# Performance work log

Hardware: AMD Instinct MI355X
Metric: run time of the kernel (lower is better)

The kernel has to match this reference:

```python
import jax, jax.numpy as jnp
import numpy as np

NUM_HEADS = 8
EPS = 1e-9


def setup_inputs() -> dict:
    key = jax.random.key(0)
    ks = jax.random.split(key, 8)
    B, N, D = 2, 2048, 512
    s = 1.0 / np.sqrt(D)
    x = jax.random.normal(ks[0], (B, N, D), dtype=jnp.float32)
    adjacency = jax.random.uniform(ks[1], (B, N, N), dtype=jnp.float32)
    # Linear weights stored as (in, out) so application is x @ W + b
    W_q = jax.random.normal(ks[2], (D, D), dtype=jnp.float32) * s
    W_k = jax.random.normal(ks[3], (D, D), dtype=jnp.float32) * s
    W_v = jax.random.normal(ks[4], (D, D), dtype=jnp.float32) * s
    b_q = jnp.zeros((D,), jnp.float32)
    b_k = jnp.zeros((D,), jnp.float32)
    b_v = jnp.zeros((D,), jnp.float32)
    # soul_gate: Linear(2D -> 1); weight stored as flat (2D,), bias scalar
    w_g = jax.random.normal(ks[5], (2 * D,), dtype=jnp.float32) * (1.0 / np.sqrt(2 * D))
    b_g = jnp.zeros((), jnp.float32)
    return {"x": x, "adjacency": adjacency, "W_q": W_q, "b_q": b_q,
            "W_k": W_k, "b_k": b_k, "W_v": W_v, "b_v": b_v,
            "w_g": w_g, "b_g": b_g}


def reference(x, adjacency, W_q, b_q, W_k, b_k, W_v, b_v, w_g, b_g):
    B, N, D = x.shape
    H = NUM_HEADS
    hd = D // H
    Q = (x @ W_q + b_q).reshape(B, N, H, hd)
    K = (x @ W_k + b_k).reshape(B, N, H, hd)
    V = (x @ W_v + b_v).reshape(B, N, H, hd)
    scores = jnp.einsum('bihd,bjhd->bhij', Q, K) / jnp.sqrt(jnp.float32(hd))
    # soul_gate(cat[x_i, x_j]) is linear, so it decomposes exactly:
    # bias[b,i,j] = x[b,i]@w_g[:D] + x[b,j]@w_g[D:] + b_g  (same math, no (B,N,N,2D) tensor)
    a = x @ w_g[:D]          # (B, N) contribution of x_i
    c = x @ w_g[D:]          # (B, N) contribution of x_j
    soul_bias = a[:, :, None] + c[:, None, :] + b_g   # (B, N, N)
    scores = scores + (soul_bias + jnp.log(adjacency + EPS))[:, None, :, :]
    attn = jax.nn.softmax(scores, axis=-1)            # (B, H, N, N)
    out = jnp.einsum('bhij,bjhd->bihd', attn, V).reshape(B, N, D)
    return out + x
```

## Files before the change

kernel.cpp:

```cpp
#include <hip/hip_runtime.h>
#include <hip/hip_bf16.h>

typedef __bf16 bf16x8 __attribute__((ext_vector_type(8)));
typedef float f32x4 __attribute__((ext_vector_type(4)));
typedef unsigned short u16x8 __attribute__((ext_vector_type(8)));

#define LOG2E 1.44269504f

__device__ __forceinline__ unsigned short f2bu(float f) {
    __hip_bfloat16 h = __float2bfloat16(f);
    unsigned short u;
    __builtin_memcpy(&u, &h, 2);
    return u;
}

__device__ __forceinline__ float fexp2(float x) {
#if __has_builtin(__builtin_amdgcn_exp2f)
    return __builtin_amdgcn_exp2f(x);
#else
    return __expf(x * 0.69314718f);
#endif
}

__device__ __forceinline__ float bu2f(unsigned short u) {
    unsigned int v = ((unsigned int)u) << 16;
    float f;
    __builtin_memcpy(&f, &v, 4);
    return f;
}

#define GLDS16(gp, lp) __builtin_amdgcn_global_load_lds( \
    (const __attribute__((address_space(1))) unsigned int*)(gp), \
    (__attribute__((address_space(3))) unsigned int*)(lp), 16, 0, 0)

#define OFF_QS  0u
#define OFF_KB  4194304u
#define OFF_VT  8388608u
#define OFF_CV  12582912u
#define OFF_XB  12599296u
#define OFF_WT  16793600u
#define OFF_MQ  18366464u
#define OFF_PO  35143680u
#define OFF_PL  51920896u

__global__ void k_prepwt(const float* __restrict__ x, const float* __restrict__ wg,
                         const float* __restrict__ w0, const float* __restrict__ w1,
                         const float* __restrict__ w2,
                         unsigned short* __restrict__ xb, float* __restrict__ cv2,
                         unsigned short* __restrict__ wt) {
    if (blockIdx.x < 1024) {
        int row = blockIdx.x * 4 + (threadIdx.x >> 6);
        int l = threadIdx.x & 63;
        const float4* xr = reinterpret_cast<const float4*>(x + (size_t)row * 512);
        float4 a = xr[l * 2], b2 = xr[l * 2 + 1];
        ushort4 o0, o1;
        o0.x = f2bu(a.x);  o0.y = f2bu(a.y);  o0.z = f2bu(a.z);  o0.w = f2bu(a.w);
        o1.x = f2bu(b2.x); o1.y = f2bu(b2.y); o1.z = f2bu(b2.z); o1.w = f2bu(b2.w);
        ushort4* dst = reinterpret_cast<ushort4*>(xb + (size_t)row * 512);
        dst[l * 2] = o0; dst[l * 2 + 1] = o1;
        const float4* wr = reinterpret_cast<const float4*>(wg + 512);
        float4 g0 = wr[l * 2], g1 = wr[l * 2 + 1];
        float s = a.x * g0.x + a.y * g0.y + a.z * g0.z + a.w * g0.w
                + b2.x * g1.x + b2.y * g1.y + b2.z * g1.z + b2.w * g1.w;
#pragma unroll
        for (int off = 32; off >= 1; off >>= 1) s += __shfl_xor(s, off, 64);
        if (l == 0) cv2[row] = fexp2((s - 8.0f) * LOG2E);
    } else {
        int bid2 = blockIdx.x - 1024;
        int z = bid2 >> 6, yy = bid2 & 63;
        int k0 = (yy >> 3) * 64, n0 = (yy & 7) * 64;
        const float* W = (z == 0) ? w0 : ((z == 1) ? w1 : w2);
        __shared__ float T[64][65];
        int c = threadIdx.x & 63, r0 = threadIdx.x >> 6;
#pragma unroll
        for (int i = 0; i < 16; i++) { int r = r0 + i * 4; T[r][c] = W[(k0 + r) * 512 + n0 + c]; }
        __syncthreads();
        unsigned short* Wt = wt + z * (512 * 512);
#pragma unroll
        for (int i = 0; i < 16; i++) { int a = r0 + i * 4; Wt[(n0 + a) * 512 + k0 + c] = f2bu(T[c][a]); }
    }
}

__global__ __launch_bounds__(256) void k_mid(
    const float* __restrict__ adj, const float* __restrict__ cv2,
    unsigned short* __restrict__ mq,
    const unsigned short* __restrict__ xb, const unsigned short* __restrict__ wt,
    const float* __restrict__ bq, const float* __restrict__ bk, const float* __restrict__ bv,
    unsigned short* __restrict__ Qs, unsigned short* __restrict__ Kb,
    unsigned short* __restrict__ Vt) {
    if (blockIdx.x < 8192) {
        int blk = blockIdx.x;
        int bic = blk >> 5, jt = blk & 31;
        int b = bic >> 7, ic = bic & 127;
        int t = threadIdx.x;
        int l = t >> 2, mt = t & 3, q = l >> 4, cl = l & 15;
        int j0 = jt * 64 + 16 * mt + q * 4;
        const float4 av = *reinterpret_cast<const float4*>(
            adj + ((size_t)(b * 2048 + ic * 16 + cl)) * 2048 + j0);
        const float4 cv = *reinterpret_cast<const float4*>(cv2 + b * 2048 + j0);
        ushort4 o;
        o.x = f2bu((av.x + 1e-9f) * cv.x);
        o.y = f2bu((av.y + 1e-9f) * cv.y);
        o.z = f2bu((av.z + 1e-9f) * cv.z);
        o.w = f2bu((av.w + 1e-9f) * cv.w);
        *reinterpret_cast<ushort4*>(mq + (size_t)bic * 32768 + jt * 1024 + l * 16 + mt * 4) = o;
        return;
    }
    int gid = blockIdx.x - 8192;
    int bx = gid & 63, by = (gid >> 6) & 3, z = gid >> 8;
    __shared__ __align__(16) unsigned short As[64 * 32];
    __shared__ __align__(16) unsigned short Bs[128 * 32];
    const unsigned short* Wt = wt + z * (512 * 512);
    const float* bias = (z == 0) ? bq : ((z == 1) ? bk : bv);
    float scale = (z == 0) ? (0.125f * LOG2E) : 1.0f;
    int m0 = bx * 64, n0 = by * 128;
    int tid = threadIdx.x, w = tid >> 6, l = tid & 63;
    int q = l >> 4, cl = l & 15;
    f32x4 acc[8];
#pragma unroll
    for (int nt = 0; nt < 8; nt++)
#pragma unroll
        for (int r = 0; r < 4; r++) acc[nt][r] = 0.f;
    int arow = l >> 2, ach = (l & 3) * 8;
    for (int k0 = 0; k0 < 512; k0 += 32) {
        GLDS16(xb + (size_t)(m0 + w * 16 + arow) * 512 + k0 + ach, As + w * 512);
#pragma unroll
        for (int e = 0; e < 2; e++)
            GLDS16(Wt + (size_t)(n0 + w * 32 + e * 16 + arow) * 512 + k0 + ach, Bs + w * 1024 + e * 512);
        __syncthreads();
        bf16x8 af = *reinterpret_cast<const bf16x8*>(As + (w * 16 + cl) * 32 + q * 8);
#pragma unroll
        for (int nt = 0; nt < 8; nt++) {
            bf16x8 bf = *reinterpret_cast<const bf16x8*>(Bs + (nt * 16 + cl) * 32 + q * 8);
            acc[nt] = __builtin_amdgcn_mfma_f32_16x16x32_bf16(af, bf, acc[nt], 0, 0, 0);
        }
        __syncthreads();
    }
    if (z == 2) {
        int n_ = (m0 + w * 16 + q * 4) & 2047;
        int b_ = (m0 + w * 16) >> 11;
#pragma unroll
        for (int nt = 0; nt < 8; nt++) {
            int col = n0 + nt * 16 + cl;
            int h_ = col >> 6, d_ = col & 63;
            float bv_ = bias[col];
            ushort4 o;
            o.x = f2bu(acc[nt][0] + bv_); o.y = f2bu(acc[nt][1] + bv_);
            o.z = f2bu(acc[nt][2] + bv_); o.w = f2bu(acc[nt][3] + bv_);
            *reinterpret_cast<ushort4*>(Vt + ((size_t)((b_ * 8 + h_) * 64 + d_)) * 2048 + n_) = o;
        }
    } else {
        unsigned short* Cout = (z == 0) ? Qs : Kb;
#pragma unroll
        for (int nt = 0; nt < 8; nt++) {
            int col = n0 + nt * 16 + cl;
            float bv_ = bias[col];
#pragma unroll
            for (int r = 0; r < 4; r++) {
                int row = m0 + w * 16 + q * 4 + r;
                Cout[(size_t)row * 512 + col] = f2bu((acc[nt][r] + bv_) * scale);
            }
        }
    }
}

__global__ __launch_bounds__(256, 3) void k_attn(
    const unsigned short* __restrict__ Qs, const unsigned short* __restrict__ Kb,
    const unsigned short* __restrict__ Vt, const unsigned short* __restrict__ mq,
    unsigned short* __restrict__ PO, float* __restrict__ PL) {
    __shared__ __align__(16) unsigned short Ks[2][4096];
    __shared__ __align__(16) unsigned short Vs[2][4096];
    __shared__ __align__(16) unsigned short PA[4][32 * 72];
    int bid = blockIdx.x;
    int h = bid >> 7, b = (bid >> 6) & 1, ig = (bid >> 2) & 15, js = bid & 3;
    int tid = threadIdx.x, w = tid >> 6, l = tid & 63, q = l >> 4, cl = l & 15;
    int bh = b * 8 + h;
    int ic0 = ig * 8 + w * 2;

    bf16x8 qf[2][2];
#pragma unroll
    for (int rc = 0; rc < 2; rc++) {
        const unsigned short* qp = Qs + (size_t)(b * 2048 + ig * 128 + w * 32 + rc * 16 + cl) * 512 + h * 64 + q * 8;
        qf[rc][0] = *reinterpret_cast<const bf16x8*>(qp);
        qf[rc][1] = *reinterpret_cast<const bf16x8*>(qp + 32);
    }
    bf16x8 ones;
#pragma unroll
    for (int i = 0; i < 8; i++) { unsigned short o1 = 0x3F80; __builtin_memcpy(((unsigned short*)&ones) + i, &o1, 2); }

    f32x4 O[2][4];
    f32x4 Osum[2];
#pragma unroll
    for (int rc = 0; rc < 2; rc++) {
#pragma unroll
        for (int nt = 0; nt < 4; nt++)
#pragma unroll
            for (int r = 0; r < 4; r++) O[rc][nt][r] = 0.f;
#pragma unroll
        for (int r = 0; r < 4; r++) Osum[rc][r] = 0.f;
    }

    const unsigned short* Kh = Kb + (size_t)b * 2048 * 512 + h * 64;
    const unsigned short* Vh = Vt + ((size_t)bh * 64) * 2048;
    const unsigned short* mb0 = mq + (size_t)(b * 128 + ic0) * 32768 + l * 16 + (size_t)(js * 8) * 1024;
    const unsigned short* mb1 = mb0 + 32768;
    unsigned short* pw = &PA[w][0];
    int lrow = l >> 2, lch = (l & 3) * 8;
    int jb0 = js * 512;

#pragma unroll
    for (int e = 0; e < 2; e++) {
        int c = w * 2 + e, kk = c >> 2, r16 = (c & 3) * 16;
        GLDS16(Kh + (size_t)(jb0 + r16 + lrow) * 512 + kk * 32 + lch, &Ks[0][kk * 2048 + r16 * 32]);
        GLDS16(Vh + (size_t)(r16 + lrow) * 2048 + jb0 + kk * 32 + lch, &Vs[0][kk * 2048 + r16 * 32]);
    }

    for (int t = 0; t < 8; t++) {
        int bufi = t & 1;
        __syncthreads();
        if (t < 7) {
            int jb = jb0 + (t + 1) * 64;
#pragma unroll
            for (int e = 0; e < 2; e++) {
                int c = w * 2 + e, kk = c >> 2, r16 = (c & 3) * 16;
                GLDS16(Kh + (size_t)(jb + r16 + lrow) * 512 + kk * 32 + lch, &Ks[bufi ^ 1][kk * 2048 + r16 * 32]);
                GLDS16(Vh + (size_t)(r16 + lrow) * 2048 + jb + kk * 32 + lch, &Vs[bufi ^ 1][kk * 2048 + r16 * 32]);
            }
        }
        u16x8 mc[2][2];
        {
            size_t off = (size_t)t * 1024;
            mc[0][0] = *reinterpret_cast<const u16x8*>(mb0 + off);
            mc[0][1] = *reinterpret_cast<const u16x8*>(mb0 + off + 8);
            mc[1][0] = *reinterpret_cast<const u16x8*>(mb1 + off);
            mc[1][1] = *reinterpret_cast<const u16x8*>(mb1 + off + 8);
        }
        f32x4 S[2][4];
#pragma unroll
        for (int rc = 0; rc < 2; rc++)
#pragma unroll
            for (int mt = 0; mt < 4; mt++)
#pragma unroll
                for (int r = 0; r < 4; r++) S[rc][mt][r] = 0.f;
#pragma unroll
        for (int mt = 0; mt < 4; mt++) {
            bf16x8 kf0 = *reinterpret_cast<const bf16x8*>(&Ks[bufi][(16 * mt + cl) * 32 + q * 8]);
            bf16x8 kf1 = *reinterpret_cast<const bf16x8*>(&Ks[bufi][2048 + (16 * mt + cl) * 32 + q * 8]);
#pragma unroll
            for (int rc = 0; rc < 2; rc++) {
                S[rc][mt] = __builtin_amdgcn_mfma_f32_16x16x32_bf16(kf0, qf[rc][0], S[rc][mt], 0, 0, 0);
                S[rc][mt] = __builtin_amdgcn_mfma_f32_16x16x32_bf16(kf1, qf[rc][1], S[rc][mt], 0, 0, 0);
            }
        }
#pragma unroll
        for (int rc = 0; rc < 2; rc++) {
#pragma unroll
            for (int mt = 0; mt < 4; mt++) {
                float p0 = fexp2(S[rc][mt][0]) * bu2f((mt < 2) ? mc[rc][0][mt * 4 + 0] : mc[rc][1][(mt - 2) * 4 + 0]);
                float p1 = fexp2(S[rc][mt][1]) * bu2f((mt < 2) ? mc[rc][0][mt * 4 + 1] : mc[rc][1][(mt - 2) * 4 + 1]);
                float p2 = fexp2(S[rc][mt][2]) * bu2f((mt < 2) ? mc[rc][0][mt * 4 + 2] : mc[rc][1][(mt - 2) * 4 + 2]);
                float p3 = fexp2(S[rc][mt][3]) * bu2f((mt < 2) ? mc[rc][0][mt * 4 + 3] : mc[rc][1][(mt - 2) * 4 + 3]);
                ushort4 o;
                o.x = f2bu(p0); o.y = f2bu(p1); o.z = f2bu(p2); o.w = f2bu(p3);
                *reinterpret_cast<ushort4*>(pw + rc * (16 * 72) + cl * 72 + 16 * mt + q * 4) = o;
            }
        }
#pragma unroll
        for (int jc = 0; jc < 2; jc++) {
            bf16x8 pf0 = *reinterpret_cast<const bf16x8*>(pw + cl * 72 + jc * 32 + q * 8);
            bf16x8 pf1 = *reinterpret_cast<const bf16x8*>(pw + 16 * 72 + cl * 72 + jc * 32 + q * 8);
#pragma unroll
            for (int nt = 0; nt < 4; nt++) {
                bf16x8 vf = *reinterpret_cast<const bf16x8*>(&Vs[bufi][jc * 2048 + (16 * nt + cl) * 32 + q * 8]);
                O[0][nt] = __builtin_amdgcn_mfma_f32_16x16x32_bf16(pf0, vf, O[0][nt], 0, 0, 0);
                O[1][nt] = __builtin_amdgcn_mfma_f32_16x16x32_bf16(pf1, vf, O[1][nt], 0, 0, 0);
            }
            Osum[0] = __builtin_amdgcn_mfma_f32_16x16x32_bf16(pf0, ones, Osum[0], 0, 0, 0);
            Osum[1] = __builtin_amdgcn_mfma_f32_16x16x32_bf16(pf1, ones, Osum[1], 0, 0, 0);
        }
    }

#pragma unroll
    for (int rc = 0; rc < 2; rc++) {
        size_t chunk = ((size_t)(bh * 128 + ic0 + rc)) * 4 + js;
        unsigned short* po = PO + chunk * 1024 + l * 16;
#pragma unroll
        for (int r = 0; r < 4; r++) {
            ushort4 o;
            o.x = f2bu(O[rc][0][r]); o.y = f2bu(O[rc][1][r]);
            o.z = f2bu(O[rc][2][r]); o.w = f2bu(O[rc][3][r]);
            *reinterpret_cast<ushort4*>(po + r * 4) = o;
        }
        if (cl == 0) {
#pragma unroll
            for (int r = 0; r < 4; r++)
                PL[chunk * 16 + q * 4 + r] = Osum[rc][r];
        }
    }
}

__global__ void k_comb(const unsigned short* __restrict__ PO, const float* __restrict__ PL,
                       const float* __restrict__ x, float* __restrict__ out) {
    int blk = blockIdx.x;
    int t64 = blk & 31, bh = blk >> 5;
    int b = bh >> 3, h = bh & 7;
    int t = threadIdx.x;
    int l = t >> 2, r = t & 3, q = l >> 4, cl = l & 15;
#pragma unroll
    for (int w = 0; w < 4; w++) {
        int ic = t64 * 4 + w;
        size_t c0 = ((size_t)(bh * 128 + ic)) * 4;
        float o0 = 0.f, o1 = 0.f, o2 = 0.f, o3 = 0.f, lsum = 0.f;
#pragma unroll
        for (int js = 0; js < 4; js++) {
            ushort4 a = *reinterpret_cast<const ushort4*>(PO + (c0 + js) * 1024 + t * 4);
            o0 += bu2f(a.x); o1 += bu2f(a.y); o2 += bu2f(a.z); o3 += bu2f(a.w);
            lsum += PL[(c0 + js) * 16 + q * 4 + r];
        }
        float inv = 1.0f / lsum;
        size_t gro = (size_t)(b * 2048 + ic * 16 + q * 4 + r) * 512 + h * 64;
        out[gro + 0 * 16 + cl] = o0 * inv + x[gro + 0 * 16 + cl];
        out[gro + 1 * 16 + cl] = o1 * inv + x[gro + 1 * 16 + cl];
        out[gro + 2 * 16 + cl] = o2 * inv + x[gro + 2 * 16 + cl];
        out[gro + 3 * 16 + cl] = o3 * inv + x[gro + 3 * 16 + cl];
    }
}

extern "C" void kernel_launch(void* const* d_in, const int* in_sizes, int n_in,
                              void* d_out, int out_size, void* d_ws, size_t ws_size,
                              hipStream_t stream) {
    const float* x   = (const float*)d_in[0];
    const float* adj = (const float*)d_in[1];
    const float* Wq  = (const float*)d_in[2];
    const float* bq  = (const float*)d_in[3];
    const float* Wk  = (const float*)d_in[4];
    const float* bk  = (const float*)d_in[5];
    const float* Wv  = (const float*)d_in[6];
    const float* bv  = (const float*)d_in[7];
    const float* wg  = (const float*)d_in[8];
    float* out = (float*)d_out;
    char* ws = (char*)d_ws;
    unsigned short* Qs = (unsigned short*)(ws + OFF_QS);
    unsigned short* Kb = (unsigned short*)(ws + OFF_KB);
    unsigned short* Vt = (unsigned short*)(ws + OFF_VT);
    float* cv2 = (float*)(ws + OFF_CV);
    unsigned short* xb = (unsigned short*)(ws + OFF_XB);
    unsigned short* wt = (unsigned short*)(ws + OFF_WT);
    unsigned short* mqp = (unsigned short*)(ws + OFF_MQ);
    unsigned short* PO = (unsigned short*)(ws + OFF_PO);
    float* PL = (float*)(ws + OFF_PL);

    k_prepwt<<<1216, 256, 0, stream>>>(x, wg, Wq, Wk, Wv, xb, cv2, wt);
    k_mid<<<8960, 256, 0, stream>>>(adj, cv2, mqp, xb, wt, bq, bk, bv, Qs, Kb, Vt);
    k_attn<<<1024, 256, 0, stream>>>(Qs, Kb, Vt, mqp, PO, PL);
    k_comb<<<512, 256, 0, stream>>>(PO, PL, x, out);
}
```

Before: 156.8 us.

## Retile QKV GEMM to 128x128, prefetch mask tiles and prioritize MFMA in attention

The QKV projection blocks move from 64x128 tiles to 128x128 tiles with a 2x2 wave layout, which raises fragment reuse per LDS read. These blocks are also moved ahead of the adjacency/mask conversion blocks in the launch order. The attention loop is unrolled by two with ping-pong mask registers, so the next tile's mask values load during the current tile's compute. MFMA sections are wrapped in s_setprio, and the partial-output store is widened to 16-byte vectors. The trade-off is higher register pressure in both kernels, which may hurt occupancy under the existing launch bounds.

```diff
diff --git a/kernel.cpp b/kernel.cpp
--- a/kernel.cpp
+++ b/kernel.cpp
@@ -88,8 +88,8 @@
     const float* __restrict__ bq, const float* __restrict__ bk, const float* __restrict__ bv,
     unsigned short* __restrict__ Qs, unsigned short* __restrict__ Kb,
     unsigned short* __restrict__ Vt) {
-    if (blockIdx.x < 8192) {
-        int blk = blockIdx.x;
+    if (blockIdx.x >= 384) {
+        int blk = blockIdx.x - 384;
         int bic = blk >> 5, jt = blk & 31;
         int b = bic >> 7, ic = bic & 127;
         int t = threadIdx.x;
@@ -106,61 +106,75 @@
         *reinterpret_cast<ushort4*>(mq + (size_t)bic * 32768 + jt * 1024 + l * 16 + mt * 4) = o;
         return;
     }
-    int gid = blockIdx.x - 8192;
-    int bx = gid & 63, by = (gid >> 6) & 3, z = gid >> 8;
-    __shared__ __align__(16) unsigned short As[64 * 32];
+    int gid = blockIdx.x;
+    int bx = gid & 31, by = (gid >> 5) & 3, z = gid >> 7;
+    __shared__ __align__(16) unsigned short As[128 * 32];
     __shared__ __align__(16) unsigned short Bs[128 * 32];
     const unsigned short* Wt = wt + z * (512 * 512);
     const float* bias = (z == 0) ? bq : ((z == 1) ? bk : bv);
     float scale = (z == 0) ? (0.125f * LOG2E) : 1.0f;
-    int m0 = bx * 64, n0 = by * 128;
+    int m0 = bx * 128, n0 = by * 128;
     int tid = threadIdx.x, w = tid >> 6, l = tid & 63;
     int q = l >> 4, cl = l & 15;
-    f32x4 acc[8];
-#pragma unroll
-    for (int nt = 0; nt < 8; nt++)
-#pragma unroll
-        for (int r = 0; r < 4; r++) acc[nt][r] = 0.f;
+    int wr = w >> 1, wc = w & 1;
+    f32x4 acc[4][4];
+#pragma unroll
+    for (int mi = 0; mi < 4; mi++)
+#pragma unroll
+        for (int ni = 0; ni < 4; ni++)
+#pragma unroll
+            for (int r = 0; r < 4; r++) acc[mi][ni][r] = 0.f;
     int arow = l >> 2, ach = (l & 3) * 8;
     for (int k0 = 0; k0 < 512; k0 += 32) {
-        GLDS16(xb + (size_t)(m0 + w * 16 + arow) * 512 + k0 + ach, As + w * 512);
-#pragma unroll
-        for (int e = 0; e < 2; e++)
-            GLDS16(Wt + (size_t)(n0 + w * 32 + e * 16 + arow) * 512 + k0 + ach, Bs + w * 1024 + e * 512);
+#pragma unroll
+        for (int e = 0; e < 2; e++) {
+            GLDS16(xb + (size_t)(m0 + w * 32 + e * 16 + arow) * 512 + k0 + ach, As + (w * 32 + e * 16) * 32);
+            GLDS16(Wt + (size_t)(n0 + w * 32 + e * 16 + arow) * 512 + k0 + ach, Bs + (w * 32 + e * 16) * 32);
+        }
         __syncthreads();
-        bf16x8 af = *reinterpret_cast<const bf16x8*>(As + (w * 16 + cl) * 32 + q * 8);
-#pragma unroll
-        for (int nt = 0; nt < 8; nt++) {
-            bf16x8 bf = *reinterpret_cast<const bf16x8*>(Bs + (nt * 16 + cl) * 32 + q * 8);
-            acc[nt] = __builtin_amdgcn_mfma_f32_16x16x32_bf16(af, bf, acc[nt], 0, 0, 0);
-        }
+        bf16x8 af[4], bfr[4];
+#pragma unroll
+        for (int i = 0; i < 4; i++) {
+            af[i]  = *reinterpret_cast<const bf16x8*>(As + (wr * 64 + i * 16 + cl) * 32 + q * 8);
+            bfr[i] = *reinterpret_cast<const bf16x8*>(Bs + (wc * 64 + i * 16 + cl) * 32 + q * 8);
+        }
+#pragma unroll
+        for (int mi = 0; mi < 4; mi++)
+#pragma unroll
+            for (int ni = 0; ni < 4; ni++)
+                acc[mi][ni] = __builtin_amdgcn_mfma_f32_16x16x32_bf16(af[mi], bfr[ni], acc[mi][ni], 0, 0, 0);
         __syncthreads();
     }
     if (z == 2) {
-        int n_ = (m0 + w * 16 + q * 4) & 2047;
-        int b_ = (m0 + w * 16) >> 11;
-#pragma unroll
-        for (int nt = 0; nt < 8; nt++) {
-            int col = n0 + nt * 16 + cl;
-            int h_ = col >> 6, d_ = col & 63;
-            float bv_ = bias[col];
-            ushort4 o;
-            o.x = f2bu(acc[nt][0] + bv_); o.y = f2bu(acc[nt][1] + bv_);
-            o.z = f2bu(acc[nt][2] + bv_); o.w = f2bu(acc[nt][3] + bv_);
-            *reinterpret_cast<ushort4*>(Vt + ((size_t)((b_ * 8 + h_) * 64 + d_)) * 2048 + n_) = o;
+        int b_ = (m0 + wr * 64) >> 11;
+#pragma unroll
+        for (int mi = 0; mi < 4; mi++) {
+            int n_ = (m0 + wr * 64 + mi * 16 + q * 4) & 2047;
+#pragma unroll
+            for (int ni = 0; ni < 4; ni++) {
+                int col = n0 + wc * 64 + ni * 16 + cl;
+                int h_ = col >> 6, d_ = col & 63;
+                float bv_ = bias[col];
+                ushort4 o;
+                o.x = f2bu(acc[mi][ni][0] + bv_); o.y = f2bu(acc[mi][ni][1] + bv_);
+                o.z = f2bu(acc[mi][ni][2] + bv_); o.w = f2bu(acc[mi][ni][3] + bv_);
+                *reinterpret_cast<ushort4*>(Vt + ((size_t)((b_ * 8 + h_) * 64 + d_)) * 2048 + n_) = o;
+            }
         }
     } else {
         unsigned short* Cout = (z == 0) ? Qs : Kb;
 #pragma unroll
-        for (int nt = 0; nt < 8; nt++) {
-            int col = n0 + nt * 16 + cl;
-            float bv_ = bias[col];
-#pragma unroll
-            for (int r = 0; r < 4; r++) {
-                int row = m0 + w * 16 + q * 4 + r;
-                Cout[(size_t)row * 512 + col] = f2bu((acc[nt][r] + bv_) * scale);
+        for (int mi = 0; mi < 4; mi++)
+#pragma unroll
+            for (int ni = 0; ni < 4; ni++) {
+                int col = n0 + wc * 64 + ni * 16 + cl;
+                float bv_ = bias[col];
+#pragma unroll
+                for (int r = 0; r < 4; r++) {
+                    int row = m0 + wr * 64 + mi * 16 + q * 4 + r;
+                    Cout[(size_t)row * 512 + col] = f2bu((acc[mi][ni][r] + bv_) * scale);
+                }
             }
-        }
     }
 }
 
@@ -214,83 +228,102 @@
         GLDS16(Kh + (size_t)(jb0 + r16 + lrow) * 512 + kk * 32 + lch, &Ks[0][kk * 2048 + r16 * 32]);
         GLDS16(Vh + (size_t)(r16 + lrow) * 2048 + jb0 + kk * 32 + lch, &Vs[0][kk * 2048 + r16 * 32]);
     }
-
-    for (int t = 0; t < 8; t++) {
-        int bufi = t & 1;
-        __syncthreads();
-        if (t < 7) {
-            int jb = jb0 + (t + 1) * 64;
-#pragma unroll
-            for (int e = 0; e < 2; e++) {
-                int c = w * 2 + e, kk = c >> 2, r16 = (c & 3) * 16;
-                GLDS16(Kh + (size_t)(jb + r16 + lrow) * 512 + kk * 32 + lch, &Ks[bufi ^ 1][kk * 2048 + r16 * 32]);
-                GLDS16(Vh + (size_t)(r16 + lrow) * 2048 + jb + kk * 32 + lch, &Vs[bufi ^ 1][kk * 2048 + r16 * 32]);
-            }
-        }
-        u16x8 mc[2][2];
-        {
-            size_t off = (size_t)t * 1024;
-            mc[0][0] = *reinterpret_cast<const u16x8*>(mb0 + off);
-            mc[0][1] = *reinterpret_cast<const u16x8*>(mb0 + off + 8);
-            mc[1][0] = *reinterpret_cast<const u16x8*>(mb1 + off);
-            mc[1][1] = *reinterpret_cast<const u16x8*>(mb1 + off + 8);
-        }
-        f32x4 S[2][4];
-#pragma unroll
-        for (int rc = 0; rc < 2; rc++)
-#pragma unroll
-            for (int mt = 0; mt < 4; mt++)
-#pragma unroll
-                for (int r = 0; r < 4; r++) S[rc][mt][r] = 0.f;
-#pragma unroll
-        for (int mt = 0; mt < 4; mt++) {
-            bf16x8 kf0 = *reinterpret_cast<const bf16x8*>(&Ks[bufi][(16 * mt + cl) * 32 + q * 8]);
-            bf16x8 kf1 = *reinterpret_cast<const bf16x8*>(&Ks[bufi][2048 + (16 * mt + cl) * 32 + q * 8]);
-#pragma unroll
-            for (int rc = 0; rc < 2; rc++) {
-                S[rc][mt] = __builtin_amdgcn_mfma_f32_16x16x32_bf16(kf0, qf[rc][0], S[rc][mt], 0, 0, 0);
-                S[rc][mt] = __builtin_amdgcn_mfma_f32_16x16x32_bf16(kf1, qf[rc][1], S[rc][mt], 0, 0, 0);
-            }
-        }
-#pragma unroll
-        for (int rc = 0; rc < 2; rc++) {
-#pragma unroll
-            for (int mt = 0; mt < 4; mt++) {
-                float p0 = fexp2(S[rc][mt][0]) * bu2f((mt < 2) ? mc[rc][0][mt * 4 + 0] : mc[rc][1][(mt - 2) * 4 + 0]);
-                float p1 = fexp2(S[rc][mt][1]) * bu2f((mt < 2) ? mc[rc][0][mt * 4 + 1] : mc[rc][1][(mt - 2) * 4 + 1]);
-                float p2 = fexp2(S[rc][mt][2]) * bu2f((mt < 2) ? mc[rc][0][mt * 4 + 2] : mc[rc][1][(mt - 2) * 4 + 2]);
-                float p3 = fexp2(S[rc][mt][3]) * bu2f((mt < 2) ? mc[rc][0][mt * 4 + 3] : mc[rc][1][(mt - 2) * 4 + 3]);
-                ushort4 o;
-                o.x = f2bu(p0); o.y = f2bu(p1); o.z = f2bu(p2); o.w = f2bu(p3);
-                *reinterpret_cast<ushort4*>(pw + rc * (16 * 72) + cl * 72 + 16 * mt + q * 4) = o;
-            }
-        }
-#pragma unroll
-        for (int jc = 0; jc < 2; jc++) {
-            bf16x8 pf0 = *reinterpret_cast<const bf16x8*>(pw + cl * 72 + jc * 32 + q * 8);
-            bf16x8 pf1 = *reinterpret_cast<const bf16x8*>(pw + 16 * 72 + cl * 72 + jc * 32 + q * 8);
-#pragma unroll
-            for (int nt = 0; nt < 4; nt++) {
-                bf16x8 vf = *reinterpret_cast<const bf16x8*>(&Vs[bufi][jc * 2048 + (16 * nt + cl) * 32 + q * 8]);
-                O[0][nt] = __builtin_amdgcn_mfma_f32_16x16x32_bf16(pf0, vf, O[0][nt], 0, 0, 0);
-                O[1][nt] = __builtin_amdgcn_mfma_f32_16x16x32_bf16(pf1, vf, O[1][nt], 0, 0, 0);
-            }
-            Osum[0] = __builtin_amdgcn_mfma_f32_16x16x32_bf16(pf0, ones, Osum[0], 0, 0, 0);
-            Osum[1] = __builtin_amdgcn_mfma_f32_16x16x32_bf16(pf1, ones, Osum[1], 0, 0, 0);
-        }
-    }
-
+    u16x8 mcA[2][2], mcB[2][2];
+    mcA[0][0] = *reinterpret_cast<const u16x8*>(mb0);
+    mcA[0][1] = *reinterpret_cast<const u16x8*>(mb0 + 8);
+    mcA[1][0] = *reinterpret_cast<const u16x8*>(mb1);
+    mcA[1][1] = *reinterpret_cast<const u16x8*>(mb1 + 8);
+
+#define ATT_BODY(T, BUF, MCC, MCN, PRED) { \
+    __syncthreads();    \
+    if (PRED) { \
+        int jb = jb0 + ((T) + 1) * 64; \
+        _Pragma("unroll") \
+        for (int e = 0; e < 2; e++) { \
+            int c = w * 2 + e, kk = c >> 2, r16 = (c & 3) * 16; \
+            GLDS16(Kh + (size_t)(jb + r16 + lrow) * 512 + kk * 32 + lch, &Ks[(BUF) ^ 1][kk * 2048 + r16 * 32]); \
+            GLDS16(Vh + (size_t)(r16 + lrow) * 2048 + jb + kk * 32 + lch, &Vs[(BUF) ^ 1][kk * 2048 + r16 * 32]); \
+        } \
+        size_t off = (size_t)((T) + 1) * 1024; \
+        MCN[0][0] = *reinterpret_cast<const u16x8*>(mb0 + off); \
+        MCN[0][1] = *reinterpret_cast<const u16x8*>(mb0 + off + 8); \
+        MCN[1][0] = *reinterpret_cast<const u16x8*>(mb1 + off); \
+        MCN[1][1] = *reinterpret_cast<const u16x8*>(mb1 + off + 8); \
+    } \
+     \
+    f32x4 S[2][4]; \
+    _Pragma("unroll") \
+    for (int rc = 0; rc < 2; rc++) \
+        _Pragma("unroll") \
+        for (int mt = 0; mt < 4; mt++) \
+            _Pragma("unroll") \
+            for (int r = 0; r < 4; r++) S[rc][mt][r] = 0.f; \
+    __builtin_amdgcn_s_setprio(1); \
+    _Pragma("unroll") \
+    for (int mt = 0; mt < 4; mt++) { \
+        bf16x8 kf0 = *reinterpret_cast<const bf16x8*>(&Ks[BUF][(16 * mt + cl) * 32 + q * 8]); \
+        bf16x8 kf1 = *reinterpret_cast<const bf16x8*>(&Ks[BUF][2048 + (16 * mt + cl) * 32 + q * 8]); \
+        _Pragma("unroll") \
+        for (int rc = 0; rc < 2; rc++) { \
+            S[rc][mt] = __builtin_amdgcn_mfma_f32_16x16x32_bf16(kf0, qf[rc][0], S[rc][mt], 0, 0, 0); \
+            S[rc][mt] = __builtin_amdgcn_mfma_f32_16x16x32_bf16(kf1, qf[rc][1], S[rc][mt], 0, 0, 0); \
+        } \
+    } \
+    __builtin_amdgcn_s_setprio(0); \
+     \
+    _Pragma("unroll") \
+    for (int rc = 0; rc < 2; rc++) { \
+        _Pragma("unroll") \
+        for (int mt = 0; mt < 4; mt++) { \
+            float p0 = fexp2(S[rc][mt][0]) * bu2f((mt < 2) ? MCC[rc][0][mt * 4 + 0] : MCC[rc][1][(mt - 2) * 4 + 0]); \
+            float p1 = fexp2(S[rc][mt][1]) * bu2f((mt < 2) ? MCC[rc][0][mt * 4 + 1] : MCC[rc][1][(mt - 2) * 4 + 1]); \
+            float p2 = fexp2(S[rc][mt][2]) * bu2f((mt < 2) ? MCC[rc][0][mt * 4 + 2] : MCC[rc][1][(mt - 2) * 4 + 2]); \
+            float p3 = fexp2(S[rc][mt][3]) * bu2f((mt < 2) ? MCC[rc][0][mt * 4 + 3] : MCC[rc][1][(mt - 2) * 4 + 3]); \
+            ushort4 o; \
+            o.x = f2bu(p0); o.y = f2bu(p1); o.z = f2bu(p2); o.w = f2bu(p3); \
+            *reinterpret_cast<ushort4*>(pw + rc * (16 * 72) + cl * 72 + 16 * mt + q * 4) = o; \
+        } \
+    } \
+     \
+    __builtin_amdgcn_s_setprio(1); \
+    _Pragma("unroll") \
+    for (int jc = 0; jc < 2; jc++) { \
+        bf16x8 pf0 = *reinterpret_cast<const bf16x8*>(pw + cl * 72 + jc * 32 + q * 8); \
+        bf16x8 pf1 = *reinterpret_cast<const bf16x8*>(pw + 16 * 72 + cl * 72 + jc * 32 + q * 8); \
+        _Pragma("unroll") \
+        for (int nt = 0; nt < 4; nt++) { \
+            bf16x8 vf = *reinterpret_cast<const bf16x8*>(&Vs[BUF][jc * 2048 + (16 * nt + cl) * 32 + q * 8]); \
+            O[0][nt] = __builtin_amdgcn_mfma_f32_16x16x32_bf16(pf0, vf, O[0][nt], 0, 0, 0); \
+            O[1][nt] = __builtin_amdgcn_mfma_f32_16x16x32_bf16(pf1, vf, O[1][nt], 0, 0, 0); \
+        } \
+        Osum[0] = __builtin_amdgcn_mfma_f32_16x16x32_bf16(pf0, ones, Osum[0], 0, 0, 0); \
+        Osum[1] = __builtin_amdgcn_mfma_f32_16x16x32_bf16(pf1, ones, Osum[1], 0, 0, 0); \
+    } \
+    __builtin_amdgcn_s_setprio(0); \
+}
+
+    for (int tt = 0; tt < 4; tt++) {
+        int t0 = tt * 2;
+        ATT_BODY(t0, 0, mcA, mcB, 1)
+        ATT_BODY(t0 + 1, 1, mcB, mcA, (tt < 3))
+    }
+#undef ATT_BODY
+
+    typedef unsigned short u16x8s __attribute__((ext_vector_type(8)));
 #pragma unroll
     for (int rc = 0; rc < 2; rc++) {
         size_t chunk = ((size_t)(bh * 128 + ic0 + rc)) * 4 + js;
         unsigned short* po = PO + chunk * 1024 + l * 16;
-#pragma unroll
-        for (int r = 0; r < 4; r++) {
-            ushort4 o;
-            o.x = f2bu(O[rc][0][r]); o.y = f2bu(O[rc][1][r]);
-            o.z = f2bu(O[rc][2][r]); o.w = f2bu(O[rc][3][r]);
-            *reinterpret_cast<ushort4*>(po + r * 4) = o;
-        }
+        u16x8s o01, o23;
+#pragma unroll
+        for (int nt = 0; nt < 4; nt++) {
+            o01[nt]     = f2bu(O[rc][nt][0]);
+            o01[4 + nt] = f2bu(O[rc][nt][1]);
+            o23[nt]     = f2bu(O[rc][nt][2]);
+            o23[4 + nt] = f2bu(O[rc][nt][3]);
+        }
+        *reinterpret_cast<u16x8s*>(po) = o01;
+        *reinterpret_cast<u16x8s*>(po + 8) = o23;
         if (cl == 0) {
 #pragma unroll
             for (int r = 0; r < 4; r++)
@@ -351,7 +384,7 @@
     float* PL = (float*)(ws + OFF_PL);
 
     k_prepwt<<<1216, 256, 0, stream>>>(x, wg, Wq, Wk, Wv, xb, cv2, wt);
-    k_mid<<<8960, 256, 0, stream>>>(adj, cv2, mqp, xb, wt, bq, bk, bv, Qs, Kb, Vt);
+    k_mid<<<8576, 256, 0, stream>>>(adj, cv2, mqp, xb, wt, bq, bk, bv, Qs, Kb, Vt);
     k_attn<<<1024, 256, 0, stream>>>(Qs, Kb, Vt, mqp, PO, PL);
     k_comb<<<512, 256, 0, stream>>>(PO, PL, x, out);
 }
```

Result: faster. 151.5 us (-3.3%).
